# Kernel tuning notes

Hardware: AMD Instinct MI355X
Metric: run time of the kernel (lower is better)

The kernel has to match this reference:

```python
import jax, jax.numpy as jnp
import numpy as np

B, S, D = 32, 257, 1024
H, HD = 16, 64
E, R, K = 8, 16, 2
SCALE = HD ** -0.5


def _lora_linear(x, w_fixed, A_all, B_all, bias, idx, gates):
    # x: [B,S,D]; w_fixed: [O,D]; A_all: [E,R,D]; B_all: [E,O,R]; idx: [B,K]; gates: [B,K]
    base = jnp.einsum('bsd,od->bso', x, w_fixed)
    A_sel = A_all[idx]  # [B,K,R,D] per-sample expert gather
    B_sel = B_all[idx]  # [B,K,O,R]
    xa = jnp.einsum('bsd,bkrd->bksr', x, A_sel)          # low-rank down-proj
    expert = jnp.einsum('bksr,bkor,bk->bso', xa, B_sel, gates)
    return base + expert + bias


def setup_inputs() -> dict:
    key = jax.random.key(0)
    ks = jax.random.split(key, 20)
    inp = {
        'hidden_states': jax.random.normal(ks[0], (B, S, D), jnp.float32),
        'top_k_indices': jax.random.randint(ks[1], (B, K), 0, E),
        'top_k_gates': jax.random.uniform(ks[2], (B, K), jnp.float32),
    }
    i = 3
    for name in ('q', 'k', 'v', 'o'):
        inp[f'w{name}_fixed'] = jax.random.normal(ks[i], (D, D), jnp.float32) * 0.02; i += 1
        inp[f'A_{name}'] = jax.random.normal(ks[i], (E, R, D), jnp.float32) * 0.02; i += 1
        inp[f'B_{name}'] = jax.random.normal(ks[i], (E, D, R), jnp.float32) * 0.02; i += 1
        inp[f'b_{name}'] = jnp.zeros((D,), jnp.float32)
    return inp


def reference(hidden_states, top_k_indices, top_k_gates,
              wq_fixed, A_q, B_q, b_q,
              wk_fixed, A_k, B_k, b_k,
              wv_fixed, A_v, B_v, b_v,
              wo_fixed, A_o, B_o, b_o):
    idx, gates = top_k_indices, top_k_gates
    q = _lora_linear(hidden_states, wq_fixed, A_q, B_q, b_q, idx, gates) * SCALE
    k = _lora_linear(hidden_states, wk_fixed, A_k, B_k, b_k, idx, gates)
    v = _lora_linear(hidden_states, wv_fixed, A_v, B_v, b_v, idx, gates)
    # [B,S,D] -> [B,H,S,HD]
    q = q.reshape(B, S, H, HD).transpose(0, 2, 1, 3)
    k = k.reshape(B, S, H, HD).transpose(0, 2, 1, 3)
    v = v.reshape(B, S, H, HD).transpose(0, 2, 1, 3)
    attn = jax.nn.softmax(jnp.einsum('bhsd,bhtd->bhst', q, k), axis=-1)
    out = jnp.einsum('bhst,bhtd->bhsd', attn, v)
    out = out.transpose(0, 2, 1, 3).reshape(B, S, D)
    return _lora_linear(out, wo_fixed, A_o, B_o, b_o, idx, gates)
```

## Files before the change

kernel.cpp:

```cpp
#include <hip/hip_runtime.h>


#define BB 32
#define SS 257
#define DD 1024
#define HH 16
#define HDIM 64
#define EE 8
#define RR 16
#define MTOT (BB * SS)
#define MPAD 8448
#define VTS 264

typedef __attribute__((ext_vector_type(8))) _Float16 f16x8;
typedef __attribute__((ext_vector_type(4))) float f32x4;

static __device__ __forceinline__ float4 ld4(const float* p) {
    return *(const float4*)p;
}
static __device__ __forceinline__ unsigned short f16b(float x) {
    union { _Float16 f; unsigned short u; } cv;
    cv.f = (_Float16)x;
    return cv.u;
}

static __device__ __forceinline__ void gl_lds16(const unsigned short* g,
                                                unsigned short* l) {
    __builtin_amdgcn_global_load_lds(
        (const __attribute__((address_space(1))) unsigned int*)g,
        (__attribute__((address_space(3))) unsigned int*)l, 16, 0, 0);
}

__global__ __launch_bounds__(256) void prep(
    const float* __restrict__ hidden, const float* __restrict__ wq,
    const float* __restrict__ wk, const float* __restrict__ wv,
    const float* __restrict__ wo, const float* __restrict__ Aq,
    const float* __restrict__ Ak, const float* __restrict__ Av,
    const float* __restrict__ Ao, const float* __restrict__ Bq,
    const float* __restrict__ Bk, const float* __restrict__ Bv,
    const float* __restrict__ Bo, const int* __restrict__ tki,
    const float* __restrict__ tkg, unsigned short* __restrict__ Xf,
    unsigned short* __restrict__ Wcat, unsigned short* __restrict__ Who,
    unsigned short* __restrict__ A3, unsigned short* __restrict__ Ao16,
    unsigned short* __restrict__ Bccat, unsigned short* __restrict__ Bco)
{
    const int tid = threadIdx.x;
    int bx = blockIdx.x;
    if (bx < 8448) {
        long i = ((long)bx * 256 + tid) * 4;
        float4 v = (i < (long)MTOT * DD) ? ld4(&hidden[i])
                                         : make_float4(0.f, 0.f, 0.f, 0.f);
        ushort4 hv;
        hv.x = f16b(v.x); hv.y = f16b(v.y); hv.z = f16b(v.z); hv.w = f16b(v.w);
        *(ushort4*)&Xf[i] = hv;
        return;
    }
    bx -= 8448;
    if (bx < 4096) {
        const int sel = bx >> 10;
        long i = ((long)(bx & 1023) * 256 + tid) * 4;
        const float* src = (sel == 0) ? wq : (sel == 1) ? wk
                                          : (sel == 2) ? wv : wo;
        unsigned short* dst =
            (sel < 3) ? Wcat + (size_t)sel * DD * DD : Who;
        float4 v = ld4(&src[i]);
        ushort4 hv;
        hv.x = f16b(v.x); hv.y = f16b(v.y); hv.z = f16b(v.z); hv.w = f16b(v.w);
        *(ushort4*)&dst[i] = hv;
        return;
    }
    bx -= 4096;
    if (bx < 512) {
        const int sel = bx >> 7;
        long i = ((long)(bx & 127) * 256 + tid) * 4;
        const float* src = (sel == 0) ? Aq : (sel == 1) ? Ak
                                          : (sel == 2) ? Av : Ao;
        unsigned short* dst =
            (sel < 3) ? A3 + (size_t)sel * EE * RR * DD : Ao16;
        float4 v = ld4(&src[i]);
        ushort4 hv;
        hv.x = f16b(v.x); hv.y = f16b(v.y); hv.z = f16b(v.z); hv.w = f16b(v.w);
        *(ushort4*)&dst[i] = hv;
        return;
    }
    bx -= 512;
    {
        const int set = bx >> 8;
        const int i = (bx & 255) * 256 + tid;
        const int b = i >> 11;
        const int rem = i & 2047;
        const int n = rem >> 1;
        const int ke = rem & 1;
        const float* Ball = (set == 0) ? Bq : (set == 1) ? Bk
                                           : (set == 2) ? Bv : Bo;
        const int e = tki[b * 2 + ke];
        const float g = tkg[b * 2 + ke];
        const float* sp = &Ball[((size_t)e * DD + n) * RR];
        unsigned short o16[16];
#pragma unroll
        for (int r4 = 0; r4 < 4; ++r4) {
            float4 v = ld4(sp + r4 * 4);
            o16[r4 * 4 + 0] = f16b(g * v.x);
            o16[r4 * 4 + 1] = f16b(g * v.y);
            o16[r4 * 4 + 2] = f16b(g * v.z);
            o16[r4 * 4 + 3] = f16b(g * v.w);
        }
        unsigned short* dst =
            (set < 3) ? &Bccat[((size_t)b * 3072 + set * 1024 + n) * 32 + ke * 16]
                      : &Bco[((size_t)b * 1024 + n) * 32 + ke * 16];
        *(uint4*)&dst[0] = *(uint4*)&o16[0];
        *(uint4*)&dst[8] = *(uint4*)&o16[8];
    }
}

#define COMPUTE1()                                                             \
    do {                                                                       \
        f16x8 af[4], bf[4];                                                    \
        const int sb = (quad ^ ((l16 >> 1) & 3)) * 8;                          \
        _Pragma("unroll") for (int t = 0; t < 4; ++t) {                        \
            af[t] = *(const f16x8*)&Ah[(wm + t * 16 + l16) * 32 + sb];         \
            bf[t] = *(const f16x8*)&Bh[(wn + t * 16 + l16) * 32 + sb];         \
        }                                                                      \
        _Pragma("unroll") for (int i = 0; i < 4; ++i)                          \
        _Pragma("unroll") for (int j = 0; j < 4; ++j)                          \
            acc[i][j] = __builtin_amdgcn_mfma_f32_16x16x32_f16(                \
                af[i], bf[j], acc[i][j], 0, 0, 0);                             \
    } while (0)

__global__ __launch_bounds__(256) void gemm_xa(
    const unsigned short* __restrict__ Xf, const unsigned short* __restrict__ A0,
    const unsigned short* __restrict__ A1, const unsigned short* __restrict__ A2,
    unsigned short* __restrict__ XA, int ncols)
{
    __shared__ unsigned short Ah[128 * 32];
    __shared__ unsigned short Bh[128 * 32];
    const int tid = threadIdx.x;
    const int m0 = blockIdx.y * 128;
    const int p = blockIdx.x;
    const unsigned short* Ap = (p == 0) ? A0 : (p == 1) ? A1 : A2;
    const int lane = tid & 63;
    const int w = tid >> 6;
    const int wm = (w >> 1) * 64;
    const int wn = (w & 1) * 64;
    const int l16 = lane & 15;
    const int quad = lane >> 4;

    f32x4 acc[4][4];
#pragma unroll
    for (int i = 0; i < 4; ++i)
#pragma unroll
        for (int j = 0; j < 4; ++j) acc[i][j] = (f32x4){0.f, 0.f, 0.f, 0.f};

    const int srow = tid >> 2;
    const int scol = (((tid & 3) ^ ((tid >> 3) & 3))) * 8;
    const int lbase = (tid & 192) * 8;
    const size_t xr0 = (size_t)(m0 + srow) * DD + scol;
    const size_t xr1 = (size_t)(m0 + srow + 64) * DD + scol;
    const size_t ar0 = (size_t)srow * DD + scol;
    const size_t ar1 = (size_t)(srow + 64) * DD + scol;

#pragma unroll 1
    for (int kt = 0; kt < 32; ++kt) {
        const int k0 = kt * 32;
        gl_lds16(Xf + xr0 + k0, &Ah[lbase]);
        gl_lds16(Xf + xr1 + k0, &Ah[2048 + lbase]);
        gl_lds16(Ap + ar0 + k0, &Bh[lbase]);
        gl_lds16(Ap + ar1 + k0, &Bh[2048 + lbase]);
        __syncthreads();
        COMPUTE1();
        __syncthreads();
    }

#pragma unroll
    for (int j = 0; j < 4; ++j) {
        const int col = p * 128 + wn + j * 16 + l16;
#pragma unroll
        for (int i = 0; i < 4; ++i) {
            const int mb = m0 + wm + i * 16 + quad * 4;
#pragma unroll
            for (int rg = 0; rg < 4; ++rg) {
                const int m = mb + rg;
                if (m < MTOT)
                    XA[(size_t)m * ncols + col] = f16b(acc[i][j][rg]);
            }
        }
    }
}

#define QKV_STAGE(BUFI, KT)                                                    \
    do {                                                                       \
        unsigned short* dA_ = S + (BUFI) * 16384 + w * 512;                    \
        const int k0_ = (KT) * 32;                                             \
        gl_lds16(Xf + gA + k0_, dA_);                                          \
        gl_lds16(Wcat + gB + k0_, dA_ + 8192);                                 \
    } while (0)

#define QKV_PHASES(BUFI)                                                       \
    do {                                                                       \
        const unsigned short* Ab_ = S + (BUFI) * 16384;                        \
        const unsigned short* Bb_ = Ab_ + 8192;                                \
        f16x8 af_[4], bf_[4];                                                  \
        _Pragma("unroll") for (int j = 0; j < 4; ++j)                          \
            bf_[j] = *(const f16x8*)&Bb_[boff + j * 512];                      \
        _Pragma("unroll") for (int i = 0; i < 4; ++i)                          \
            af_[i] = *(const f16x8*)&Ab_[aoff + i * 512];                      \
        __builtin_amdgcn_s_setprio(1);                                         \
        _Pragma("unroll") for (int i = 0; i < 4; ++i)                          \
        _Pragma("unroll") for (int j = 0; j < 4; ++j)                          \
            acc[i][j] = __builtin_amdgcn_mfma_f32_16x16x32_f16(                \
                af_[i], bf_[j], acc[i][j], 0, 0, 0);                           \
        __builtin_amdgcn_s_setprio(0);                                         \
    } while (0)

__global__ __launch_bounds__(1024)
__attribute__((amdgpu_waves_per_eu(4, 4))) void gemm_qkv(
    const unsigned short* __restrict__ Xf, const unsigned short* __restrict__ Wcat,
    const float* __restrict__ bq, const float* __restrict__ bk,
    const float* __restrict__ bv, const unsigned short* __restrict__ XAd,
    const unsigned short* __restrict__ Bccat, const int* __restrict__ idx,
    unsigned short* __restrict__ qh, unsigned short* __restrict__ kh,
    unsigned short* __restrict__ vTg)
{
    __shared__ unsigned short S[65536];
    const int tid = threadIdx.x;
    const int bxn = blockIdx.x;
    const int m0 = blockIdx.y * 256;
    const int p = bxn >> 2;
    const int n0g = bxn * 256;
    const int nloc0 = (bxn & 3) * 256;
    const int lane = tid & 63;
    const int w = tid >> 6;
    const int wm = (w >> 2) * 64;
    const int wn = (w & 3) * 64;
    const int l16 = lane & 15;
    const int quad = lane >> 4;
    const int sb = (quad ^ ((l16 >> 1) & 3)) * 8;
    const int aoff = (wm + l16) * 32 + sb;
    const int boff = (wn + l16) * 32 + sb;

    f32x4 acc[4][4];
#pragma unroll
    for (int i = 0; i < 4; ++i)
#pragma unroll
        for (int j = 0; j < 4; ++j) acc[i][j] = (f32x4){0.f, 0.f, 0.f, 0.f};

    const int srow = tid >> 2;
    const int schk = ((tid & 3) ^ ((srow >> 1) & 3)) * 8;
    const size_t gA = (size_t)(m0 + srow) * DD + schk;
    const size_t gB = (size_t)(n0g + srow) * DD + schk;

    QKV_STAGE(0, 0);
    QKV_STAGE(1, 1);
    QKV_STAGE(2, 2);
#pragma unroll 1
    for (int kt = 0; kt < 30; ++kt) {
        asm volatile("s_waitcnt vmcnt(4)\n\ts_barrier" ::: "memory");
        if (kt < 29) QKV_STAGE((kt + 3) & 3, kt + 3);
        QKV_PHASES(kt & 3);
    }
    asm volatile("s_waitcnt vmcnt(2)\n\ts_barrier" ::: "memory");
    QKV_PHASES(2);
    asm volatile("s_waitcnt vmcnt(0)\n\ts_barrier" ::: "memory");
    QKV_PHASES(3);

    {
        int m_hi = m0 + 255;
        if (m_hi >= MTOT) m_hi = MTOT - 1;
        const int b_first = m0 / SS;
        const int b_last = m_hi / SS;
        const int r = tid >> 2;
        const int cc = tid & 3;
        const int key = (r >> 1) & 3;
        const int g = cc ^ key;
        const uint4 z = make_uint4(0, 0, 0, 0);
#pragma unroll 1
        for (int bp = b_first; bp <= b_last; ++bp) {
            const int gm = m0 + r;
            const bool va = (gm < MTOT) && (gm / SS == bp);
            uint4 av = z;
            if (va) {
                const int e = idx[bp * 2 + (g >> 1)];
                av = *(const uint4*)&XAd[(size_t)gm * 384 + p * 128 +
                                         e * 16 + (g & 1) * 8];
            }
            const size_t bo = ((size_t)bp * 3072 + p * 1024 + nloc0 + r) * 32;
            uint4 bv2 = *(const uint4*)&Bccat[bo + g * 8];
            __syncthreads();
            *(uint4*)&S[r * 32 + cc * 8] = av;
            *(uint4*)&S[8192 + r * 32 + cc * 8] = bv2;
            __syncthreads();
            QKV_PHASES(0);
            __syncthreads();
        }
    }

    unsigned short* Epi = S;
    const float* bias = (p == 0) ? bq : (p == 1) ? bk : bv;
    if (p < 2) {
        const float alpha = (p == 0) ? 0.125f : 1.0f;
        unsigned short* C = (p == 0) ? qh : kh;
#pragma unroll 1
        for (int half = 0; half < 2; ++half) {
            if ((w >> 3) == half) {
#pragma unroll
                for (int j = 0; j < 4; ++j) {
                    const int col = wn + j * 16 + l16;
                    const float bvl = bias[nloc0 + col];
                    const int lm0 = wm - half * 128;
#pragma unroll
                    for (int i = 0; i < 4; ++i) {
                        const int ml = lm0 + i * 16 + quad * 4;
#pragma unroll
                        for (int rg = 0; rg < 4; ++rg)
                            Epi[(ml + rg) * 264 + col] =
                                f16b(alpha * (acc[i][j][rg] + bvl));
                    }
                }
            }
            __syncthreads();
            {
                const int r = tid >> 3;
                const int c = (tid & 7) * 32;
                const int m = m0 + half * 128 + r;
                if (m < MTOT) {
#pragma unroll
                    for (int k = 0; k < 4; ++k)
                        *(uint4*)&C[(size_t)m * DD + nloc0 + c + k * 8] =
                            *(const uint4*)&Epi[r * 264 + c + k * 8];
                }
            }
            __syncthreads();
        }
    } else {
#pragma unroll 1
        for (int hh = 0; hh < 4; ++hh) {
            if ((w >> 2) == hh) {
#pragma unroll
                for (int j = 0; j < 4; ++j) {
                    const int col = wn + j * 16 + l16;
                    const float bvl = bias[nloc0 + col];
#pragma unroll
                    for (int i = 0; i < 4; ++i) {
                        const int ml = i * 16 + quad * 4;
                        ushort4 pk;
                        pk.x = f16b(acc[i][j][0] + bvl);
                        pk.y = f16b(acc[i][j][1] + bvl);
                        pk.z = f16b(acc[i][j][2] + bvl);
                        pk.w = f16b(acc[i][j][3] + bvl);
                        *(ushort4*)&Epi[col * 68 + ml] = pk;
                    }
                }
            }
            __syncthreads();
            {
                const int tl = tid & 63;
                const int mg = m0 + hh * 64 + tl;
                if (mg < MTOT) {
                    const int bq2 = mg / SS;
                    const int t = mg - bq2 * SS;
#pragma unroll 4
                    for (int k = 0; k < 16; ++k) {
                        const int nll = (tid >> 6) + k * 16;
                        const int d = nloc0 + nll;
                        vTg[((size_t)(bq2 * HH + (d >> 6)) * HDIM + (d & 63)) *
                                VTS + t] = Epi[nll * 68 + tl];
                    }
                }
            }
            __syncthreads();
        }
    }
}

__global__ __launch_bounds__(256) void gemm_o(
    const unsigned short* __restrict__ Xf, const unsigned short* __restrict__ Wh2,
    const float* __restrict__ bias, const unsigned short* __restrict__ XAo,
    const unsigned short* __restrict__ Bco, const int* __restrict__ idx,
    float* __restrict__ Cf)
{
    __shared__ unsigned short Ah[128 * 32];
    __shared__ unsigned short Bh[128 * 32];
    const int tid = threadIdx.x;
    const int m0 = blockIdx.y * 128;
    const int n0 = blockIdx.x * 128;
    const int lane = tid & 63;
    const int w = tid >> 6;
    const int wm = (w >> 1) * 64;
    const int wn = (w & 1) * 64;
    const int l16 = lane & 15;
    const int quad = lane >> 4;

    f32x4 acc[4][4];
#pragma unroll
    for (int i = 0; i < 4; ++i)
#pragma unroll
        for (int j = 0; j < 4; ++j) acc[i][j] = (f32x4){0.f, 0.f, 0.f, 0.f};

    const int srow = tid >> 2;
    const int scol = (((tid & 3) ^ ((tid >> 3) & 3))) * 8;
    const int lbase = (tid & 192) * 8;
    const size_t xr0 = (size_t)(m0 + srow) * DD + scol;
    const size_t xr1 = (size_t)(m0 + srow + 64) * DD + scol;
    const size_t wr0 = (size_t)(n0 + srow) * DD + scol;
    const size_t wr1 = (size_t)(n0 + srow + 64) * DD + scol;

#pragma unroll 1
    for (int kt = 0; kt < 32; ++kt) {
        const int k0 = kt * 32;
        gl_lds16(Xf + xr0 + k0, &Ah[lbase]);
        gl_lds16(Xf + xr1 + k0, &Ah[2048 + lbase]);
        gl_lds16(Wh2 + wr0 + k0, &Bh[lbase]);
        gl_lds16(Wh2 + wr1 + k0, &Bh[2048 + lbase]);
        __syncthreads();
        COMPUTE1();
        __syncthreads();
    }

    {
        int m_hi = m0 + 127;
        if (m_hi >= MTOT) m_hi = MTOT - 1;
        const int b_first = m0 / SS;
        const int b_last = m_hi / SS;
        const int r = tid >> 1;
        const int key = (r >> 1) & 3;
        const int b0 = (tid & 1) * 2;
        const uint4 z = make_uint4(0, 0, 0, 0);
#pragma unroll 1
        for (int bp = b_first; bp <= b_last; ++bp) {
            const int gm = m0 + r;
            const bool va = (gm < MTOT) && (gm / SS == bp);
            const int g0 = b0 ^ key, g1 = (b0 + 1) ^ key;
            uint4 av0 = z, av1 = z;
            if (va) {
                const int e0 = idx[bp * 2 + (g0 >> 1)];
                const int e1 = idx[bp * 2 + (g1 >> 1)];
                av0 = *(const uint4*)&XAo[(size_t)gm * 128 + e0 * 16 +
                                          (g0 & 1) * 8];
                av1 = *(const uint4*)&XAo[(size_t)gm * 128 + e1 * 16 +
                                          (g1 & 1) * 8];
            }
            const size_t bo = ((size_t)bp * 1024 + n0 + r) * 32;
            uint4 bv0 = *(const uint4*)&Bco[bo + g0 * 8];
            uint4 bv1 = *(const uint4*)&Bco[bo + g1 * 8];
            __syncthreads();
            *(uint4*)&Ah[r * 32 + b0 * 8] = av0;
            *(uint4*)&Ah[r * 32 + (b0 + 1) * 8] = av1;
            *(uint4*)&Bh[r * 32 + b0 * 8] = bv0;
            *(uint4*)&Bh[r * 32 + (b0 + 1) * 8] = bv1;
            __syncthreads();
            COMPUTE1();
            __syncthreads();
        }
    }

#pragma unroll
    for (int j = 0; j < 4; ++j) {
        const int n = n0 + wn + j * 16 + l16;
        const float bvl = bias[n];
#pragma unroll
        for (int i = 0; i < 4; ++i) {
            const int mb = m0 + wm + i * 16 + quad * 4;
#pragma unroll
            for (int rg = 0; rg < 4; ++rg) {
                const int m = mb + rg;
                if (m < MTOT) Cf[(size_t)m * DD + n] = acc[i][j][rg] + bvl;
            }
        }
    }
}

__global__ __launch_bounds__(512, 1) void attn_v4(
    const unsigned short* __restrict__ qh, const unsigned short* __restrict__ kh,
    const unsigned short* __restrict__ vT, unsigned short* __restrict__ Xf)
{
    __shared__ unsigned short Ks[288 * 64];
    __shared__ unsigned short Vt[64 * VTS];
    __shared__ unsigned short Qs[64 * 64];
    __shared__ unsigned short Ps[64 * 296];
    __shared__ float sredm[2][64];
    __shared__ float sreds[2][64];

    const int tid = threadIdx.x;
    const int h = blockIdx.x, b = blockIdx.y;
    const int cb = h * HDIM;
    const int lane = tid & 63;
    const int w = tid >> 6;
    const int r0 = (w & 3) * 16;
    const int ch = w >> 2;
    const int l16 = lane & 15;
    const int quad = lane >> 4;

    const size_t kbase = (size_t)(b * SS) * DD + cb;
    {
        const int rr = w * 8 + (lane >> 3);
        const int cg = ((lane & 7) ^ (rr & 7)) * 8;
#pragma unroll
        for (int c = 0; c < 4; ++c)
            gl_lds16(kh + kbase + (size_t)(c * 64 + rr) * DD + cg,
                     &Ks[(c * 64 + w * 8) * 64]);
    }
    if (tid < 256) {
        uint4 z = make_uint4(0, 0, 0, 0);
        if (tid < 8) z = *(const uint4*)&kh[kbase + (size_t)256 * DD + tid * 8];
        *(uint4*)&Ks[256 * 64 + tid * 8] = z;
    }
    {
        const size_t vbase = (size_t)(b * HH + h) * HDIM * VTS;
        for (int i = tid; i < 64 * 33; i += 512) {
            const int r = i / 33;
            const int c = i - r * 33;
            uint4 v = *(const uint4*)&vT[vbase + (size_t)r * VTS + c * 8];
            if (c == 32) { v.x &= 0xFFFFu; v.y = 0; v.z = 0; v.w = 0; }
            *(uint4*)&Vt[r * VTS + c * 8] = v;
        }
    }

#pragma unroll 1
    for (int qt = 0; qt < 5; ++qt) {
        const int s0 = qt * 64;
        __syncthreads();
        {
            int sg = s0 + (tid >> 3);
            if (sg > SS - 1) sg = SS - 1;
            const int cg = ((tid & 7) ^ ((tid >> 3) & 7)) * 8;
            gl_lds16(qh + (size_t)(b * SS + sg) * DD + cb + cg,
                     &Qs[(w * 8) * 64]);
        }
        __syncthreads();

        f32x4 lac[9];
#pragma unroll
        for (int ct = 0; ct < 9; ++ct) lac[ct] = (f32x4){0.f, 0.f, 0.f, 0.f};
#pragma unroll
        for (int kc = 0; kc < 2; ++kc) {
            const int sb = ((kc * 4 + quad) ^ (l16 & 7)) * 8;
            f16x8 af = *(const f16x8*)&Qs[(r0 + l16) * 64 + sb];
#pragma unroll
            for (int ct = 0; ct < 9; ++ct) {
                const int c0 = ch * 144 + ct * 16;
                f16x8 bf = *(const f16x8*)&Ks[(c0 + l16) * 64 + sb];
                lac[ct] = __builtin_amdgcn_mfma_f32_16x16x32_f16(
                    af, bf, lac[ct], 0, 0, 0);
            }
        }
#pragma unroll
        for (int ct = 0; ct < 9; ++ct) {
            const int t = ch * 144 + ct * 16 + l16;
            if (t > SS - 1) {
                lac[ct][0] = -1e30f; lac[ct][1] = -1e30f;
                lac[ct][2] = -1e30f; lac[ct][3] = -1e30f;
            }
        }
        float mx[4] = {-1e30f, -1e30f, -1e30f, -1e30f};
#pragma unroll
        for (int ct = 0; ct < 9; ++ct)
#pragma unroll
            for (int i = 0; i < 4; ++i) mx[i] = fmaxf(mx[i], lac[ct][i]);
#pragma unroll
        for (int o = 1; o < 16; o <<= 1)
#pragma unroll
            for (int i = 0; i < 4; ++i)
                mx[i] = fmaxf(mx[i], __shfl_xor(mx[i], o, 16));
        if (l16 == 0)
#pragma unroll
            for (int i = 0; i < 4; ++i) sredm[ch][r0 + quad * 4 + i] = mx[i];
        __syncthreads();
#pragma unroll
        for (int i = 0; i < 4; ++i)
            mx[i] = fmaxf(mx[i], sredm[1 - ch][r0 + quad * 4 + i]);
        float sm[4] = {0.f, 0.f, 0.f, 0.f};
#pragma unroll
        for (int ct = 0; ct < 9; ++ct)
#pragma unroll
            for (int i = 0; i < 4; ++i) {
                float pv = __expf(lac[ct][i] - mx[i]);
                lac[ct][i] = pv;
                sm[i] += pv;
            }
#pragma unroll
        for (int o = 1; o < 16; o <<= 1)
#pragma unroll
            for (int i = 0; i < 4; ++i) sm[i] += __shfl_xor(sm[i], o, 16);
        if (l16 == 0)
#pragma unroll
            for (int i = 0; i < 4; ++i) sreds[ch][r0 + quad * 4 + i] = sm[i];
        __syncthreads();
        float inv[4];
#pragma unroll
        for (int i = 0; i < 4; ++i)
            inv[i] = 1.f / (sm[i] + sreds[1 - ch][r0 + quad * 4 + i]);
#pragma unroll
        for (int ct = 0; ct < 9; ++ct) {
            const int col = ch * 144 + ct * 16 + l16;
#pragma unroll
            for (int i = 0; i < 4; ++i)
                Ps[(r0 + quad * 4 + i) * 296 + col] =
                    f16b(lac[ct][i] * inv[i]);
        }
        __syncthreads();

        f32x4 oacc[2];
        oacc[0] = (f32x4){0.f, 0.f, 0.f, 0.f};
        oacc[1] = (f32x4){0.f, 0.f, 0.f, 0.f};
#pragma unroll
        for (int tt = 0; tt < 9; ++tt) {
            const int t0 = tt * 32;
            f16x8 pf = *(const f16x8*)&Ps[(r0 + l16) * 296 + t0 + quad * 8];
#pragma unroll
            for (int dt = 0; dt < 2; ++dt) {
                f16x8 bvv = *(const f16x8*)&Vt[(ch * 32 + dt * 16 + l16) * VTS +
                                               t0 + quad * 8];
                oacc[dt] = __builtin_amdgcn_mfma_f32_16x16x32_f16(
                    pf, bvv, oacc[dt], 0, 0, 0);
            }
        }
#pragma unroll
        for (int dt = 0; dt < 2; ++dt)
#pragma unroll
            for (int i = 0; i < 4; ++i) {
                const int srow = s0 + r0 + quad * 4 + i;
                if (srow < SS)
                    Xf[(size_t)(b * SS + srow) * DD + cb + ch * 32 + dt * 16 +
                       l16] = f16b(oacc[dt][i]);
            }
    }
}

extern "C" void kernel_launch(void* const* d_in, const int* in_sizes, int n_in,
                              void* d_out, int out_size, void* d_ws,
                              size_t ws_size, hipStream_t stream)
{
    const float* hidden = (const float*)d_in[0];
    const int* tki = (const int*)d_in[1];
    const float* tkg = (const float*)d_in[2];
    const float* wq = (const float*)d_in[3];
    const float* Aq = (const float*)d_in[4];
    const float* Bq = (const float*)d_in[5];
    const float* bq = (const float*)d_in[6];
    const float* wk = (const float*)d_in[7];
    const float* Ak = (const float*)d_in[8];
    const float* Bk = (const float*)d_in[9];
    const float* bkb = (const float*)d_in[10];
    const float* wv = (const float*)d_in[11];
    const float* Av = (const float*)d_in[12];
    const float* Bv = (const float*)d_in[13];
    const float* bvb = (const float*)d_in[14];
    const float* wo = (const float*)d_in[15];
    const float* Ao = (const float*)d_in[16];
    const float* Bo = (const float*)d_in[17];
    const float* bob = (const float*)d_in[18];
    float* out = (float*)d_out;

    char* ws = (char*)d_ws;
    const size_t NW = (size_t)DD * DD;
    const size_t NA = (size_t)EE * RR * DD;
    unsigned short* Xf = (unsigned short*)ws;    ws += (size_t)MPAD * DD * 2;
    unsigned short* qh = (unsigned short*)ws;    ws += (size_t)MTOT * DD * 2;
    unsigned short* vTg = (unsigned short*)ws;   ws += (size_t)BB * HH * HDIM * VTS * 2;
    unsigned short* Wcat = (unsigned short*)ws;  ws += 3 * NW * 2;
    unsigned short* Who = (unsigned short*)ws;   ws += NW * 2;
    unsigned short* A3 = (unsigned short*)ws;    ws += 3 * NA * 2;
    unsigned short* Ao16 = (unsigned short*)ws;  ws += NA * 2;
    unsigned short* Bccat = (unsigned short*)ws; ws += (size_t)BB * 3072 * 32 * 2;
    unsigned short* Bco = (unsigned short*)ws;   ws += (size_t)BB * 1024 * 32 * 2;
    unsigned short* XAo = (unsigned short*)ws;   ws += (size_t)MTOT * 128 * 2;
    unsigned short* kh = (unsigned short*)d_out;
    unsigned short* XAd = (unsigned short*)((char*)d_out + (size_t)MTOT * DD * 2);

    prep<<<14080, 256, 0, stream>>>(hidden, wq, wk, wv, wo, Aq, Ak, Av, Ao,
                                    Bq, Bk, Bv, Bo, tki, tkg, Xf, Wcat, Who,
                                    A3, Ao16, Bccat, Bco);
    gemm_xa<<<dim3(3, 65), 256, 0, stream>>>(Xf, A3, A3 + NA, A3 + 2 * NA,
                                             XAd, 384);
    gemm_qkv<<<dim3(12, 33), 1024, 0, stream>>>(Xf, Wcat, bq, bkb, bvb, XAd,
                                                Bccat, tki, qh, kh, vTg);
    attn_v4<<<dim3(HH, BB), 512, 0, stream>>>(qh, kh, vTg, Xf);
    gemm_xa<<<dim3(1, 65), 256, 0, stream>>>(Xf, Ao16, Ao16, Ao16, XAo, 128);
    gemm_o<<<dim3(8, 65), 256, 0, stream>>>(Xf, Who, bob, XAo, Bco, tki, out);
}
```

Before: 366.0 us.

## Reuse pipelined 256x256 QKV GEMM for output projection and add XCD-aware block swizzle

The output-projection GEMM moves from a simple 128x128 single-buffered tile with 256 threads to the same 1024-thread, 256x256, 4-stage pipelined main loop used by the QKV GEMM, including its LoRA epilogue. Both GEMMs switch to a 1D grid whose block ids are remapped so that neighbouring tiles land on the same XCD, aiming for better L2 reuse. The aim is higher MFMA utilisation and less load latency exposure in gemm_o. The cost is only 132 blocks for gemm_o, which is below a full wave of CUs and may hurt occupancy. The M tail past 8224 relies on the padded Xf buffer.

```diff
diff --git a/kernel.cpp b/kernel.cpp
--- a/kernel.cpp
+++ b/kernel.cpp
@@ -29,6 +29,14 @@
     __builtin_amdgcn_global_load_lds(
         (const __attribute__((address_space(1))) unsigned int*)g,
         (__attribute__((address_space(3))) unsigned int*)l, 16, 0, 0);
+}
+
+static __device__ __forceinline__ int xcd_swz(int orig, int nwg) {
+    const int xcd = orig & 7;
+    const int lin = orig >> 3;
+    const int q = nwg >> 3;
+    const int r = nwg & 7;
+    return (xcd < r ? xcd * (q + 1) : r * (q + 1) + (xcd - r) * q) + lin;
 }
 
 __global__ __launch_bounds__(256) void prep(
@@ -212,6 +220,22 @@
         __builtin_amdgcn_s_setprio(0);                                         \
     } while (0)
 
+#define QKV_MAIN_LOOP()                                                        \
+    do {                                                                       \
+        QKV_STAGE(0, 0);                                                       \
+        QKV_STAGE(1, 1);                                                       \
+        QKV_STAGE(2, 2);                                                       \
+        _Pragma("unroll 1") for (int kt = 0; kt < 30; ++kt) {                  \
+            asm volatile("s_waitcnt vmcnt(4)\n\ts_barrier" ::: "memory");      \
+            if (kt < 29) QKV_STAGE((kt + 3) & 3, kt + 3);                      \
+            QKV_PHASES(kt & 3);                                                \
+        }                                                                      \
+        asm volatile("s_waitcnt vmcnt(2)\n\ts_barrier" ::: "memory");          \
+        QKV_PHASES(2);                                                         \
+        asm volatile("s_waitcnt vmcnt(0)\n\ts_barrier" ::: "memory");          \
+        QKV_PHASES(3);                                                         \
+    } while (0)
+
 __global__ __launch_bounds__(1024)
 __attribute__((amdgpu_waves_per_eu(4, 4))) void gemm_qkv(
     const unsigned short* __restrict__ Xf, const unsigned short* __restrict__ Wcat,
@@ -223,8 +247,9 @@
 {
     __shared__ unsigned short S[65536];
     const int tid = threadIdx.x;
-    const int bxn = blockIdx.x;
-    const int m0 = blockIdx.y * 256;
+    const int wgid = xcd_swz(blockIdx.x, 396);
+    const int bxn = wgid % 12;
+    const int m0 = (wgid / 12) * 256;
     const int p = bxn >> 2;
     const int n0g = bxn * 256;
     const int nloc0 = (bxn & 3) * 256;
@@ -249,19 +274,7 @@
     const size_t gA = (size_t)(m0 + srow) * DD + schk;
     const size_t gB = (size_t)(n0g + srow) * DD + schk;
 
-    QKV_STAGE(0, 0);
-    QKV_STAGE(1, 1);
-    QKV_STAGE(2, 2);
-#pragma unroll 1
-    for (int kt = 0; kt < 30; ++kt) {
-        asm volatile("s_waitcnt vmcnt(4)\n\ts_barrier" ::: "memory");
-        if (kt < 29) QKV_STAGE((kt + 3) & 3, kt + 3);
-        QKV_PHASES(kt & 3);
-    }
-    asm volatile("s_waitcnt vmcnt(2)\n\ts_barrier" ::: "memory");
-    QKV_PHASES(2);
-    asm volatile("s_waitcnt vmcnt(0)\n\ts_barrier" ::: "memory");
-    QKV_PHASES(3);
+    QKV_MAIN_LOOP();
 
     {
         int m_hi = m0 + 255;
@@ -372,23 +385,28 @@
     }
 }
 
-__global__ __launch_bounds__(256) void gemm_o(
+__global__ __launch_bounds__(1024)
+__attribute__((amdgpu_waves_per_eu(4, 4))) void gemm_o(
     const unsigned short* __restrict__ Xf, const unsigned short* __restrict__ Wh2,
     const float* __restrict__ bias, const unsigned short* __restrict__ XAo,
     const unsigned short* __restrict__ Bco, const int* __restrict__ idx,
     float* __restrict__ Cf)
 {
-    __shared__ unsigned short Ah[128 * 32];
-    __shared__ unsigned short Bh[128 * 32];
+    __shared__ unsigned short S[65536];
+    const unsigned short* Wcat = Wh2;
     const int tid = threadIdx.x;
-    const int m0 = blockIdx.y * 128;
-    const int n0 = blockIdx.x * 128;
+    const int wgid = xcd_swz(blockIdx.x, 132);
+    const int m0 = (wgid / 4) * 256;
+    const int n0 = (wgid % 4) * 256;
     const int lane = tid & 63;
     const int w = tid >> 6;
-    const int wm = (w >> 1) * 64;
-    const int wn = (w & 1) * 64;
+    const int wm = (w >> 2) * 64;
+    const int wn = (w & 3) * 64;
     const int l16 = lane & 15;
     const int quad = lane >> 4;
+    const int sb = (quad ^ ((l16 >> 1) & 3)) * 8;
+    const int aoff = (wm + l16) * 32 + sb;
+    const int boff = (wn + l16) * 32 + sb;
 
     f32x4 acc[4][4];
 #pragma unroll
@@ -397,58 +415,39 @@
         for (int j = 0; j < 4; ++j) acc[i][j] = (f32x4){0.f, 0.f, 0.f, 0.f};
 
     const int srow = tid >> 2;
-    const int scol = (((tid & 3) ^ ((tid >> 3) & 3))) * 8;
-    const int lbase = (tid & 192) * 8;
-    const size_t xr0 = (size_t)(m0 + srow) * DD + scol;
-    const size_t xr1 = (size_t)(m0 + srow + 64) * DD + scol;
-    const size_t wr0 = (size_t)(n0 + srow) * DD + scol;
-    const size_t wr1 = (size_t)(n0 + srow + 64) * DD + scol;
-
-#pragma unroll 1
-    for (int kt = 0; kt < 32; ++kt) {
-        const int k0 = kt * 32;
-        gl_lds16(Xf + xr0 + k0, &Ah[lbase]);
-        gl_lds16(Xf + xr1 + k0, &Ah[2048 + lbase]);
-        gl_lds16(Wh2 + wr0 + k0, &Bh[lbase]);
-        gl_lds16(Wh2 + wr1 + k0, &Bh[2048 + lbase]);
-        __syncthreads();
-        COMPUTE1();
-        __syncthreads();
-    }
+    const int schk = ((tid & 3) ^ ((srow >> 1) & 3)) * 8;
+    const size_t gA = (size_t)(m0 + srow) * DD + schk;
+    const size_t gB = (size_t)(n0 + srow) * DD + schk;
+
+    QKV_MAIN_LOOP();
 
     {
-        int m_hi = m0 + 127;
+        int m_hi = m0 + 255;
         if (m_hi >= MTOT) m_hi = MTOT - 1;
         const int b_first = m0 / SS;
         const int b_last = m_hi / SS;
-        const int r = tid >> 1;
+        const int r = tid >> 2;
+        const int cc = tid & 3;
         const int key = (r >> 1) & 3;
-        const int b0 = (tid & 1) * 2;
+        const int g = cc ^ key;
         const uint4 z = make_uint4(0, 0, 0, 0);
 #pragma unroll 1
         for (int bp = b_first; bp <= b_last; ++bp) {
             const int gm = m0 + r;
             const bool va = (gm < MTOT) && (gm / SS == bp);
-            const int g0 = b0 ^ key, g1 = (b0 + 1) ^ key;
-            uint4 av0 = z, av1 = z;
+            uint4 av = z;
             if (va) {
-                const int e0 = idx[bp * 2 + (g0 >> 1)];
-                const int e1 = idx[bp * 2 + (g1 >> 1)];
-                av0 = *(const uint4*)&XAo[(size_t)gm * 128 + e0 * 16 +
-                                          (g0 & 1) * 8];
-                av1 = *(const uint4*)&XAo[(size_t)gm * 128 + e1 * 16 +
-                                          (g1 & 1) * 8];
+                const int e = idx[bp * 2 + (g >> 1)];
+                av = *(const uint4*)&XAo[(size_t)gm * 128 + e * 16 +
+                                         (g & 1) * 8];
             }
             const size_t bo = ((size_t)bp * 1024 + n0 + r) * 32;
-            uint4 bv0 = *(const uint4*)&Bco[bo + g0 * 8];
-            uint4 bv1 = *(const uint4*)&Bco[bo + g1 * 8];
-            __syncthreads();
-            *(uint4*)&Ah[r * 32 + b0 * 8] = av0;
-            *(uint4*)&Ah[r * 32 + (b0 + 1) * 8] = av1;
-            *(uint4*)&Bh[r * 32 + b0 * 8] = bv0;
-            *(uint4*)&Bh[r * 32 + (b0 + 1) * 8] = bv1;
-            __syncthreads();
-            COMPUTE1();
+            uint4 bv2 = *(const uint4*)&Bco[bo + g * 8];
+            __syncthreads();
+            *(uint4*)&S[r * 32 + cc * 8] = av;
+            *(uint4*)&S[8192 + r * 32 + cc * 8] = bv2;
+            __syncthreads();
+            QKV_PHASES(0);
             __syncthreads();
         }
     }
@@ -672,9 +671,9 @@
                                     A3, Ao16, Bccat, Bco);
     gemm_xa<<<dim3(3, 65), 256, 0, stream>>>(Xf, A3, A3 + NA, A3 + 2 * NA,
                                              XAd, 384);
-    gemm_qkv<<<dim3(12, 33), 1024, 0, stream>>>(Xf, Wcat, bq, bkb, bvb, XAd,
-                                                Bccat, tki, qh, kh, vTg);
+    gemm_qkv<<<396, 1024, 0, stream>>>(Xf, Wcat, bq, bkb, bvb, XAd,
+                                       Bccat, tki, qh, kh, vTg);
     attn_v4<<<dim3(HH, BB), 512, 0, stream>>>(qh, kh, vTg, Xf);
     gemm_xa<<<dim3(1, 65), 256, 0, stream>>>(Xf, Ao16, Ao16, Ao16, XAo, 128);
-    gemm_o<<<dim3(8, 65), 256, 0, stream>>>(Xf, Who, bob, XAo, Bco, tki, out);
-}
+    gemm_o<<<132, 1024, 0, stream>>>(Xf, Who, bob, XAo, Bco, tki, out);
+}
```

After: 365.7 us. No clear change (-0.1%).
